# Kernel optimization log

Measured on AMD Instinct MI355X. Metric: run time of the kernel, lower is better.

The kernel has to match this reference:

```python
import math
import jax, jax.numpy as jnp
import numpy as np

NUM_EXPERTS = 8
TOP_K = 2
HIDDEN = 1024
INTER = 2816
CAPACITY_FACTOR = 2.0
T_TOKENS = 4096


def setup_inputs() -> dict:
    key = jax.random.key(0)
    k1, k2, k3, k4, k5 = jax.random.split(key, 5)
    hidden_states = jax.random.normal(k1, (T_TOKENS, HIDDEN), dtype=jnp.float32)
    # router-softmax-like affinities in (0,1)
    expert_affinities = jax.nn.softmax(
        jax.random.normal(k2, (T_TOKENS, NUM_EXPERTS), dtype=jnp.float32), axis=-1)
    expert_index = jax.random.randint(k3, (T_TOKENS, TOP_K), 0, NUM_EXPERTS, dtype=jnp.int64)
    scale = 0.02
    w_gate_up = jax.random.normal(k4, (NUM_EXPERTS, HIDDEN, 2 * INTER), dtype=jnp.float32) * scale
    w_down = jax.random.normal(k5, (NUM_EXPERTS, INTER, HIDDEN), dtype=jnp.float32) * scale
    return {
        "hidden_states": hidden_states,
        "expert_affinities": expert_affinities,
        "expert_index": expert_index,
        "w_gate_up": w_gate_up,
        "w_down": w_down,
    }


def _experts_mlp(x, w_gate_up, w_down):
    # x: (E, C, H) -> (E, C, H); GLU MLP per expert (grouped GEMM)
    gu = jnp.einsum('ech,ehf->ecf', x, w_gate_up)          # (E, C, 2I)
    gate, up = jnp.split(gu, 2, axis=-1)
    h = jax.nn.silu(gate) * up                              # (E, C, I)
    return jnp.einsum('eci,eih->ech', h, w_down)            # (E, C, H)


def reference(hidden_states, expert_affinities, expert_index, w_gate_up, w_down):
    T, H = hidden_states.shape
    E = w_gate_up.shape[0]
    K = expert_index.shape[1]
    # expert capacity C = min(T, ceil(T * top_k * capacity_factor / E))
    C = min(math.ceil(T * K * CAPACITY_FACTOR / E), T)

    expert_index = expert_index.astype(jnp.int32)
    # top_k-hot expert mask (T, E)
    expert_mask = jnp.sum(jax.nn.one_hot(expert_index, E, dtype=jnp.float32), axis=1)
    # 1-indexed position of each token within its expert (cumsum over tokens)
    pos = jnp.cumsum(expert_mask, axis=0)                   # (T, E)
    # drop tokens over capacity
    expert_mask = jnp.where(pos > C, 0.0, expert_mask)

    # mask affinities to chosen (non-dropped) experts, L1-normalize (normalize_top_k_affinities)
    aff = jnp.where(expert_mask == 0, 0.0, expert_affinities)
    aff = aff / jnp.maximum(jnp.sum(jnp.abs(aff), axis=1, keepdims=True), 1e-12)

    # flattened position within (E*C) permuted buffer; 0 marks dropped/unchosen
    offsets = jnp.arange(E, dtype=jnp.float32) * C
    pos_off = jnp.where(expert_mask == 0, 0.0, pos + offsets)  # (T, E)

    tidx = jnp.arange(T, dtype=jnp.int32)
    perm = jnp.take_along_axis(pos_off, expert_index, axis=1).astype(jnp.int32)  # (T, K), 1-indexed

    # scatter token ids into expert-aligned slots (slot 0 is the drop sink)
    vals = jnp.broadcast_to((tidx + 1)[:, None], (T, K))
    assign = jnp.zeros(E * C + 1, dtype=jnp.int32).at[perm.reshape(-1)].set(vals.reshape(-1))
    assign = assign[1:].reshape(E, C)

    perm = jnp.maximum(perm - 1, 0)      # (T, K) -> 0-indexed, dropped clamped to 0
    assign = jnp.maximum(assign - 1, 0)  # (E, C) -> 0-indexed, empty slots read token 0

    # permute -> grouped expert MLP -> combine
    x = hidden_states[assign]                               # (E, C, H)
    permuted = _experts_mlp(x, w_gate_up, w_down).reshape(E * C, H)

    out_k = permuted[perm]                                  # (T, K, H)
    aff_k = jnp.take_along_axis(aff, expert_index, axis=1)  # (T, K); 0 for dropped
    return jnp.sum(out_k * aff_k[..., None], axis=1)        # (T, H)
```

## Files before the change

### kernel.cpp

```cpp
#include <hip/hip_runtime.h>

#define T_TOK 4096
#define NEXP  8
#define HID   1024
#define INTER 2816
#define CAP   2048

typedef __attribute__((ext_vector_type(8))) short bf16x8;
typedef __attribute__((ext_vector_type(4))) float f32x4;

__device__ __forceinline__ float bf2f(unsigned short u){
  union { unsigned int i; float f; } c; c.i = ((unsigned int)u) << 16; return c.f;
}
__device__ __forceinline__ unsigned short f2bf(float f){
  union { float f; unsigned int i; } c; c.f = f;
  unsigned int x = c.i;
  unsigned int r = (x + 0x7fffu + ((x >> 16) & 1u)) >> 16;
  return (unsigned short)r;
}

__device__ __forceinline__ void gload_lds16(const void* g, void* l){
  __builtin_amdgcn_global_load_lds(
      (const __attribute__((address_space(1))) void*)g,
      (__attribute__((address_space(3))) void*)l, 16, 0, 0);
}

__global__ void routing_kernel(const int* __restrict__ eidx,
                               int* __restrict__ assign,
                               int* __restrict__ perm,
                               int* __restrict__ counts)
{
  int tid = threadIdx.x;
  for (int i = tid; i < NEXP * CAP; i += 512) assign[i] = 0;
  __syncthreads();
  int e = tid >> 6;
  int lane = tid & 63;
  int base = 0;
  for (int t0 = 0; t0 < T_TOK; t0 += 64){
    int t = t0 + lane;
    int i0 = eidx[2*t], i1 = eidx[2*t+1];
    int m = (i0 == e) + (i1 == e);
    int v = m;
    #pragma unroll
    for (int off = 1; off < 64; off <<= 1){
      int u = __shfl_up(v, off);
      if (lane >= off) v += u;
    }
    int pos = base + v;
    if (m > 0){
      bool dropped = pos > CAP;
      int slot = dropped ? -1 : (e * CAP + pos - 1);
      if (!dropped) assign[slot] = t;
      if (i0 == e) perm[2*t]   = slot;
      if (i1 == e) perm[2*t+1] = slot;
    }
    base += __shfl(v, 63);
  }
  if (lane == 0) counts[e] = base < CAP ? base : CAP;
}

__global__ void transpose_cast(const float* __restrict__ in, unsigned short* __restrict__ out,
                               int R, int Cc)
{
  __shared__ unsigned short tile[128][66];
  int e = blockIdx.z;
  const float* src = in + (size_t)e * R * Cc;
  unsigned short* dst = out + (size_t)e * R * Cc;
  int c0 = blockIdx.x * 64, r0 = blockIdx.y * 128;
  int tr = threadIdx.x >> 4, tc = threadIdx.x & 15;
  #pragma unroll
  for (int it = 0; it < 8; ++it){
    int r = it*16 + tr;
    float4 v = *(const float4*)(src + (size_t)(r0 + r) * Cc + c0 + tc*4);
    tile[r][tc*4+0] = f2bf(v.x);
    tile[r][tc*4+1] = f2bf(v.y);
    tile[r][tc*4+2] = f2bf(v.z);
    tile[r][tc*4+3] = f2bf(v.w);
  }
  __syncthreads();
  int j0 = tc * 8;
  #pragma unroll
  for (int it = 0; it < 4; ++it){
    int i = it*16 + tr;
    bf16x8 o;
    #pragma unroll
    for (int r = 0; r < 8; ++r) o[r] = (short)tile[j0 + r][i];
    *(bf16x8*)(dst + (size_t)(c0 + i) * R + r0 + j0) = o;
  }
}

__global__ void gather_kernel(const float* __restrict__ hidden,
                              const int* __restrict__ assign,
                              const int* __restrict__ counts,
                              unsigned short* __restrict__ x)
{
  int s = blockIdx.x;
  int e = s / CAP, local = s % CAP;
  if (local >= ((counts[e] + 127) & ~127)) return;
  int tok = assign[s];
  int c = threadIdx.x * 4;
  float4 v = *(const float4*)(hidden + (size_t)tok * HID + c);
  ushort4 o; o.x = f2bf(v.x); o.y = f2bf(v.y); o.z = f2bf(v.z); o.w = f2bf(v.w);
  *(ushort4*)(x + (size_t)s * HID + c) = o;
}

template<int ROWS>
__device__ __forceinline__ void stage_tile(const unsigned short* gbase, int ldk, int k0,
                                           unsigned short* lds, int lane, int wid){
  #pragma unroll
  for (int c = 0; c < ROWS/32; ++c){
    int rb = c*32 + wid*8;
    int row = rb + (lane >> 3);
    int slot = (lane & 7) ^ (row & 7);
    const char* src = (const char*)(gbase + (size_t)row * ldk + k0) + slot*16;
    gload_lds16(src, (char*)lds + rb*128);
  }
}

__device__ __forceinline__ bf16x8 lds_frag(const unsigned short* lds, int row, int kslot){
  int slot = kslot ^ (row & 7);
  return *(const bf16x8*)((const char*)lds + row*128 + slot*16);
}

template<bool SILU, int BN, int KSPLIT>
__global__ __launch_bounds__(256, 4)
void gemm_bf16(const unsigned short* __restrict__ A,
               const unsigned short* __restrict__ Bt,
               unsigned short* __restrict__ O,
               unsigned short* __restrict__ O2,
               const int* __restrict__ counts,
               int K, int Nout)
{
  const int NF = BN / 32;
  int z = blockIdx.z;
  int e = z / KSPLIT, kc = z % KSPLIT;
  int m0 = blockIdx.y * 128;
  if (m0 >= counts[e]) return;
  int n0 = blockIdx.x * BN;
  int klen = K / KSPLIT;
  int kbase = kc * klen;
  unsigned short* Op = (KSPLIT == 2 && kc == 1) ? O2 : O;

  __shared__ unsigned short Al[128*64];
  __shared__ unsigned short Bg[BN*64];
  __shared__ unsigned short Bu[SILU ? BN*64 : 64];

  int tid = threadIdx.x;
  int lane = tid & 63, wid = tid >> 6;
  int wm = wid >> 1, wn = wid & 1;
  int lo = lane & 15, hi = lane >> 4;

  size_t bstride = (size_t)(SILU ? 2*INTER : Nout) * K;
  const unsigned short* Ab  = A  + ((size_t)e * CAP + m0) * K;
  const unsigned short* Bgb = Bt + (size_t)e * bstride + (size_t)n0 * K;
  const unsigned short* Bub = Bt + (size_t)e * bstride + (size_t)(INTER + n0) * K;

  f32x4 accg[4][NF] = {};
  f32x4 accu[SILU ? 4 : 1][SILU ? NF : 1] = {};

  for (int k0 = kbase; k0 < kbase + klen; k0 += 64){
    stage_tile<128>(Ab,  K, k0, Al, lane, wid);
    stage_tile<BN>(Bgb, K, k0, Bg, lane, wid);
    if constexpr (SILU) stage_tile<BN>(Bub, K, k0, Bu, lane, wid);
    __syncthreads();
    #pragma unroll
    for (int kk = 0; kk < 64; kk += 32){
      int kslot = (kk >> 3) + hi;
      bf16x8 af[4], bg_[NF], bu_[NF];
      #pragma unroll
      for (int m = 0; m < 4; ++m) af[m] = lds_frag(Al, wm*64 + m*16 + lo, kslot);
      #pragma unroll
      for (int n = 0; n < NF; ++n) bg_[n] = lds_frag(Bg, wn*(BN/2) + n*16 + lo, kslot);
      if constexpr (SILU){
        #pragma unroll
        for (int n = 0; n < NF; ++n) bu_[n] = lds_frag(Bu, wn*(BN/2) + n*16 + lo, kslot);
      }
      #pragma unroll
      for (int m = 0; m < 4; ++m){
        #pragma unroll
        for (int n = 0; n < NF; ++n){
          accg[m][n] = __builtin_amdgcn_mfma_f32_16x16x32_bf16(af[m], bg_[n], accg[m][n], 0, 0, 0);
          if constexpr (SILU)
            accu[m][n] = __builtin_amdgcn_mfma_f32_16x16x32_bf16(af[m], bu_[n], accu[m][n], 0, 0, 0);
        }
      }
    }
    __syncthreads();
  }

  #pragma unroll
  for (int m = 0; m < 4; ++m){
    #pragma unroll
    for (int n = 0; n < NF; ++n){
      int gr = m0 + wm*64 + m*16 + hi*4;
      int gc = n0 + wn*(BN/2) + n*16 + lo;
      #pragma unroll
      for (int j = 0; j < 4; ++j){
        float v;
        if constexpr (SILU){
          float g = accg[m][n][j], u = accu[m][n][j];
          v = g / (1.f + __expf(-g)) * u;
        } else {
          v = accg[m][n][j];
        }
        Op[((size_t)e * CAP + gr + j) * Nout + gc] = f2bf(v);
      }
    }
  }
}

__global__ void combine_kernel(const unsigned short* __restrict__ p0,
                               const unsigned short* __restrict__ p1,
                               const int* __restrict__ perm,
                               const int* __restrict__ eidx,
                               const float* __restrict__ aff,
                               float* __restrict__ out)
{
  int t = blockIdx.x;
  int i0 = eidx[2*t], i1 = eidx[2*t+1];
  int q0 = perm[2*t], q1 = perm[2*t+1];
  float a0 = (q0 >= 0) ? aff[t*NEXP + i0] : 0.f;
  float a1 = (q1 >= 0) ? aff[t*NEXP + i1] : 0.f;
  float denom = (i0 == i1) ? fabsf(a0) : (fabsf(a0) + fabsf(a1));
  denom = fmaxf(denom, 1e-12f);
  float w0 = a0 / denom, w1 = a1 / denom;
  size_t s0 = (size_t)(q0 >= 0 ? q0 : 0) * HID;
  size_t s1 = (size_t)(q1 >= 0 ? q1 : 0) * HID;
  int c = threadIdx.x * 4;
  ushort4 v0a = *(const ushort4*)(p0 + s0 + c);
  ushort4 v0b = *(const ushort4*)(p1 + s0 + c);
  ushort4 v1a = *(const ushort4*)(p0 + s1 + c);
  ushort4 v1b = *(const ushort4*)(p1 + s1 + c);
  float4 o;
  o.x = w0*(bf2f(v0a.x)+bf2f(v0b.x)) + w1*(bf2f(v1a.x)+bf2f(v1b.x));
  o.y = w0*(bf2f(v0a.y)+bf2f(v0b.y)) + w1*(bf2f(v1a.y)+bf2f(v1b.y));
  o.z = w0*(bf2f(v0a.z)+bf2f(v0b.z)) + w1*(bf2f(v1a.z)+bf2f(v1b.z));
  o.w = w0*(bf2f(v0a.w)+bf2f(v0b.w)) + w1*(bf2f(v1a.w)+bf2f(v1b.w));
  *(float4*)(out + (size_t)t * HID + c) = o;
}

extern "C" void kernel_launch(void* const* d_in, const int* in_sizes, int n_in,
                              void* d_out, int out_size, void* d_ws, size_t ws_size,
                              hipStream_t stream)
{
  const float* hidden = (const float*)d_in[0];
  const float* aff    = (const float*)d_in[1];
  const int*   eidx   = (const int*)d_in[2];
  const float* wgu    = (const float*)d_in[3];
  const float* wdn    = (const float*)d_in[4];
  float* out = (float*)d_out;

  char* ws = (char*)d_ws;
  unsigned short* wt     = (unsigned short*)(ws + 0);
  unsigned short* p1     = (unsigned short*)(ws + 46137344);
  unsigned short* h      = (unsigned short*)(ws + 92274688);
  unsigned short* x      = (unsigned short*)(ws + 184549376);
  int* assign            = (int*)(ws + 218103808);
  int* perm              = (int*)(ws + 218169344);
  int* counts            = (int*)(ws + 218202112);

  routing_kernel<<<1, 512, 0, stream>>>(eidx, assign, perm, counts);
  transpose_cast<<<dim3(88, 8, 8), 256, 0, stream>>>(wgu, wt, HID, 2*INTER);
  gather_kernel<<<dim3(NEXP*CAP), 256, 0, stream>>>(hidden, assign, counts, x);
  gemm_bf16<true, 64, 1><<<dim3(44, 16, 8), 256, 0, stream>>>(x, wt, h, nullptr, counts, HID, INTER);
  transpose_cast<<<dim3(16, 22, 8), 256, 0, stream>>>(wdn, wt, INTER, HID);
  gemm_bf16<false, 128, 2><<<dim3(8, 16, 16), 256, 0, stream>>>(h, wt, x, p1, counts, INTER, HID);
  combine_kernel<<<dim3(T_TOK), 256, 0, stream>>>(x, p1, perm, eidx, aff, out);
}
```

Before: 308.4 us.

## Fuse weight transposes with gather and gate-up GEMM into combined launches

Merges the gate-up weight transpose and the token gather into a single prep launch, and runs the down-weight transpose inside the same launch as the first grouped GEMM. Separate buffers for the two transposed weights let the down-weight conversion overlap with GEMM1 instead of waiting for it. This removes two kernel launches and their serialization gaps. In exchange it needs a larger workspace, and the fused GEMM1 blocks share a grid with memory-bound transpose blocks, which may change occupancy and scheduling.

```diff
diff --git a/kernel.cpp b/kernel.cpp
--- a/kernel.cpp
+++ b/kernel.cpp
@@ -59,23 +59,19 @@
   if (lane == 0) counts[e] = base < CAP ? base : CAP;
 }
 
-__global__ void transpose_cast(const float* __restrict__ in, unsigned short* __restrict__ out,
-                               int R, int Cc)
-{
-  __shared__ unsigned short tile[128][66];
-  int e = blockIdx.z;
-  const float* src = in + (size_t)e * R * Cc;
-  unsigned short* dst = out + (size_t)e * R * Cc;
-  int c0 = blockIdx.x * 64, r0 = blockIdx.y * 128;
+__device__ __forceinline__ void do_transpose(const float* __restrict__ src,
+                                             unsigned short* __restrict__ dst,
+                                             int R, int Cc, int c0, int r0,
+                                             unsigned short* tile ){
   int tr = threadIdx.x >> 4, tc = threadIdx.x & 15;
   #pragma unroll
   for (int it = 0; it < 8; ++it){
     int r = it*16 + tr;
     float4 v = *(const float4*)(src + (size_t)(r0 + r) * Cc + c0 + tc*4);
-    tile[r][tc*4+0] = f2bf(v.x);
-    tile[r][tc*4+1] = f2bf(v.y);
-    tile[r][tc*4+2] = f2bf(v.z);
-    tile[r][tc*4+3] = f2bf(v.w);
+    tile[r*66 + tc*4+0] = f2bf(v.x);
+    tile[r*66 + tc*4+1] = f2bf(v.y);
+    tile[r*66 + tc*4+2] = f2bf(v.z);
+    tile[r*66 + tc*4+3] = f2bf(v.w);
   }
   __syncthreads();
   int j0 = tc * 8;
@@ -84,24 +80,34 @@
     int i = it*16 + tr;
     bf16x8 o;
     #pragma unroll
-    for (int r = 0; r < 8; ++r) o[r] = (short)tile[j0 + r][i];
+    for (int r = 0; r < 8; ++r) o[r] = (short)tile[(j0 + r)*66 + i];
     *(bf16x8*)(dst + (size_t)(c0 + i) * R + r0 + j0) = o;
   }
 }
 
-__global__ void gather_kernel(const float* __restrict__ hidden,
-                              const int* __restrict__ assign,
-                              const int* __restrict__ counts,
-                              unsigned short* __restrict__ x)
-{
-  int s = blockIdx.x;
-  int e = s / CAP, local = s % CAP;
-  if (local >= ((counts[e] + 127) & ~127)) return;
-  int tok = assign[s];
-  int c = threadIdx.x * 4;
-  float4 v = *(const float4*)(hidden + (size_t)tok * HID + c);
-  ushort4 o; o.x = f2bf(v.x); o.y = f2bf(v.y); o.z = f2bf(v.z); o.w = f2bf(v.w);
-  *(ushort4*)(x + (size_t)s * HID + c) = o;
+__global__ void prep_kernel(const float* __restrict__ wgu, unsigned short* __restrict__ wguT,
+                            const float* __restrict__ hidden,
+                            const int* __restrict__ assign, const int* __restrict__ counts,
+                            unsigned short* __restrict__ x)
+{
+  __shared__ unsigned short tile[128*66];
+  int b = blockIdx.x;
+  if (b < 5632){
+    int c0 = (b % 88) * 64;
+    int r0 = ((b / 88) & 7) * 128;
+    int e  = b / 704;
+    do_transpose(wgu + (size_t)e * HID * (2*INTER), wguT + (size_t)e * HID * (2*INTER),
+                 HID, 2*INTER, c0, r0, tile);
+  } else {
+    int s = b - 5632;
+    int e = s / CAP, local = s % CAP;
+    if (local >= ((counts[e] + 127) & ~127)) return;
+    int tok = assign[s];
+    int c = threadIdx.x * 4;
+    float4 v = *(const float4*)(hidden + (size_t)tok * HID + c);
+    ushort4 o; o.x = f2bf(v.x); o.y = f2bf(v.y); o.z = f2bf(v.z); o.w = f2bf(v.w);
+    *(ushort4*)(x + (size_t)s * HID + c) = o;
+  }
 }
 
 template<int ROWS>
@@ -122,67 +128,137 @@
   return *(const bf16x8*)((const char*)lds + row*128 + slot*16);
 }
 
-template<bool SILU, int BN, int KSPLIT>
+__device__ void gemm1_body(const unsigned short* __restrict__ A,
+                           const unsigned short* __restrict__ Bt,
+                           unsigned short* __restrict__ O,
+                           const int* __restrict__ counts,
+                           int nx, int my, int e, unsigned short* smem)
+{
+  int m0 = my * 128;
+  if (m0 >= counts[e]) return;
+  int n0 = nx * 64;
+  unsigned short* Al = smem;
+  unsigned short* Bg = smem + 8192;
+  unsigned short* Bu = smem + 12288;
+
+  int tid = threadIdx.x, lane = tid & 63, wid = tid >> 6;
+  int wm = wid >> 1, wn = wid & 1;
+  int lo = lane & 15, hi = lane >> 4;
+
+  const unsigned short* Ab  = A  + ((size_t)e * CAP + m0) * HID;
+  const unsigned short* Bgb = Bt + (size_t)e * (2*INTER) * HID + (size_t)n0 * HID;
+  const unsigned short* Bub = Bt + (size_t)e * (2*INTER) * HID + (size_t)(INTER + n0) * HID;
+
+  f32x4 accg[4][2] = {}, accu[4][2] = {};
+
+  for (int k0 = 0; k0 < HID; k0 += 64){
+    stage_tile<128>(Ab,  HID, k0, Al, lane, wid);
+    stage_tile<64>(Bgb, HID, k0, Bg, lane, wid);
+    stage_tile<64>(Bub, HID, k0, Bu, lane, wid);
+    __syncthreads();
+    #pragma unroll
+    for (int kk = 0; kk < 64; kk += 32){
+      int kslot = (kk >> 3) + hi;
+      bf16x8 af[4], bg_[2], bu_[2];
+      #pragma unroll
+      for (int m = 0; m < 4; ++m) af[m] = lds_frag(Al, wm*64 + m*16 + lo, kslot);
+      #pragma unroll
+      for (int n = 0; n < 2; ++n){
+        bg_[n] = lds_frag(Bg, wn*32 + n*16 + lo, kslot);
+        bu_[n] = lds_frag(Bu, wn*32 + n*16 + lo, kslot);
+      }
+      #pragma unroll
+      for (int m = 0; m < 4; ++m){
+        #pragma unroll
+        for (int n = 0; n < 2; ++n){
+          accg[m][n] = __builtin_amdgcn_mfma_f32_16x16x32_bf16(af[m], bg_[n], accg[m][n], 0, 0, 0);
+          accu[m][n] = __builtin_amdgcn_mfma_f32_16x16x32_bf16(af[m], bu_[n], accu[m][n], 0, 0, 0);
+        }
+      }
+    }
+    __syncthreads();
+  }
+
+  #pragma unroll
+  for (int m = 0; m < 4; ++m){
+    #pragma unroll
+    for (int n = 0; n < 2; ++n){
+      int gr = m0 + wm*64 + m*16 + hi*4;
+      int gc = n0 + wn*32 + n*16 + lo;
+      #pragma unroll
+      for (int j = 0; j < 4; ++j){
+        float g = accg[m][n][j], u = accu[m][n][j];
+        float v = g / (1.f + __expf(-g)) * u;
+        O[((size_t)e * CAP + gr + j) * INTER + gc] = f2bf(v);
+      }
+    }
+  }
+}
+
 __global__ __launch_bounds__(256, 4)
-void gemm_bf16(const unsigned short* __restrict__ A,
-               const unsigned short* __restrict__ Bt,
-               unsigned short* __restrict__ O,
-               unsigned short* __restrict__ O2,
-               const int* __restrict__ counts,
-               int K, int Nout)
-{
-  const int NF = BN / 32;
+void gemm1_wdnT(const unsigned short* __restrict__ x, const unsigned short* __restrict__ wguT,
+                unsigned short* __restrict__ h, const int* __restrict__ counts,
+                const float* __restrict__ wdn, unsigned short* __restrict__ wdT)
+{
+  __shared__ unsigned short smem[16384];
+  int b = blockIdx.x;
+  if (b < 2816){
+    int c0 = (b % 16) * 64;
+    int r0 = ((b / 16) % 22) * 128;
+    int e  = b / 352;
+    do_transpose(wdn + (size_t)e * INTER * HID, wdT + (size_t)e * INTER * HID,
+                 INTER, HID, c0, r0, smem);
+  } else {
+    int g = b - 2816;
+    int nx = g % 44, my = (g / 44) & 15, e = g / 704;
+    gemm1_body(x, wguT, h, counts, nx, my, e, smem);
+  }
+}
+
+__global__ __launch_bounds__(256, 4)
+void gemm2(const unsigned short* __restrict__ A,
+           const unsigned short* __restrict__ Bt,
+           unsigned short* __restrict__ O,
+           unsigned short* __restrict__ O2,
+           const int* __restrict__ counts)
+{
   int z = blockIdx.z;
-  int e = z / KSPLIT, kc = z % KSPLIT;
+  int e = z >> 1, kc = z & 1;
   int m0 = blockIdx.y * 128;
   if (m0 >= counts[e]) return;
-  int n0 = blockIdx.x * BN;
-  int klen = K / KSPLIT;
-  int kbase = kc * klen;
-  unsigned short* Op = (KSPLIT == 2 && kc == 1) ? O2 : O;
+  int n0 = blockIdx.x * 128;
+  int kbase = kc * (INTER/2);
+  unsigned short* Op = kc ? O2 : O;
 
   __shared__ unsigned short Al[128*64];
-  __shared__ unsigned short Bg[BN*64];
-  __shared__ unsigned short Bu[SILU ? BN*64 : 64];
-
-  int tid = threadIdx.x;
-  int lane = tid & 63, wid = tid >> 6;
+  __shared__ unsigned short Bg[128*64];
+
+  int tid = threadIdx.x, lane = tid & 63, wid = tid >> 6;
   int wm = wid >> 1, wn = wid & 1;
   int lo = lane & 15, hi = lane >> 4;
 
-  size_t bstride = (size_t)(SILU ? 2*INTER : Nout) * K;
-  const unsigned short* Ab  = A  + ((size_t)e * CAP + m0) * K;
-  const unsigned short* Bgb = Bt + (size_t)e * bstride + (size_t)n0 * K;
-  const unsigned short* Bub = Bt + (size_t)e * bstride + (size_t)(INTER + n0) * K;
-
-  f32x4 accg[4][NF] = {};
-  f32x4 accu[SILU ? 4 : 1][SILU ? NF : 1] = {};
-
-  for (int k0 = kbase; k0 < kbase + klen; k0 += 64){
-    stage_tile<128>(Ab,  K, k0, Al, lane, wid);
-    stage_tile<BN>(Bgb, K, k0, Bg, lane, wid);
-    if constexpr (SILU) stage_tile<BN>(Bub, K, k0, Bu, lane, wid);
+  const unsigned short* Ab  = A  + ((size_t)e * CAP + m0) * INTER;
+  const unsigned short* Bgb = Bt + (size_t)e * HID * INTER + (size_t)n0 * INTER;
+
+  f32x4 accg[4][4] = {};
+
+  for (int k0 = kbase; k0 < kbase + INTER/2; k0 += 64){
+    stage_tile<128>(Ab,  INTER, k0, Al, lane, wid);
+    stage_tile<128>(Bgb, INTER, k0, Bg, lane, wid);
     __syncthreads();
     #pragma unroll
     for (int kk = 0; kk < 64; kk += 32){
       int kslot = (kk >> 3) + hi;
-      bf16x8 af[4], bg_[NF], bu_[NF];
+      bf16x8 af[4], bg_[4];
       #pragma unroll
       for (int m = 0; m < 4; ++m) af[m] = lds_frag(Al, wm*64 + m*16 + lo, kslot);
       #pragma unroll
-      for (int n = 0; n < NF; ++n) bg_[n] = lds_frag(Bg, wn*(BN/2) + n*16 + lo, kslot);
-      if constexpr (SILU){
-        #pragma unroll
-        for (int n = 0; n < NF; ++n) bu_[n] = lds_frag(Bu, wn*(BN/2) + n*16 + lo, kslot);
-      }
+      for (int n = 0; n < 4; ++n) bg_[n] = lds_frag(Bg, wn*64 + n*16 + lo, kslot);
       #pragma unroll
       for (int m = 0; m < 4; ++m){
         #pragma unroll
-        for (int n = 0; n < NF; ++n){
+        for (int n = 0; n < 4; ++n)
           accg[m][n] = __builtin_amdgcn_mfma_f32_16x16x32_bf16(af[m], bg_[n], accg[m][n], 0, 0, 0);
-          if constexpr (SILU)
-            accu[m][n] = __builtin_amdgcn_mfma_f32_16x16x32_bf16(af[m], bu_[n], accu[m][n], 0, 0, 0);
-        }
       }
     }
     __syncthreads();
@@ -191,20 +267,12 @@
   #pragma unroll
   for (int m = 0; m < 4; ++m){
     #pragma unroll
-    for (int n = 0; n < NF; ++n){
+    for (int n = 0; n < 4; ++n){
       int gr = m0 + wm*64 + m*16 + hi*4;
-      int gc = n0 + wn*(BN/2) + n*16 + lo;
-      #pragma unroll
-      for (int j = 0; j < 4; ++j){
-        float v;
-        if constexpr (SILU){
-          float g = accg[m][n][j], u = accu[m][n][j];
-          v = g / (1.f + __expf(-g)) * u;
-        } else {
-          v = accg[m][n][j];
-        }
-        Op[((size_t)e * CAP + gr + j) * Nout + gc] = f2bf(v);
-      }
+      int gc = n0 + wn*64 + n*16 + lo;
+      #pragma unroll
+      for (int j = 0; j < 4; ++j)
+        Op[((size_t)e * CAP + gr + j) * HID + gc] = f2bf(accg[m][n][j]);
     }
   }
 }
@@ -251,19 +319,18 @@
   float* out = (float*)d_out;
 
   char* ws = (char*)d_ws;
-  unsigned short* wt     = (unsigned short*)(ws + 0);
-  unsigned short* p1     = (unsigned short*)(ws + 46137344);
-  unsigned short* h      = (unsigned short*)(ws + 92274688);
-  unsigned short* x      = (unsigned short*)(ws + 184549376);
-  int* assign            = (int*)(ws + 218103808);
-  int* perm              = (int*)(ws + 218169344);
-  int* counts            = (int*)(ws + 218202112);
+  unsigned short* wguT = (unsigned short*)(ws + 0);
+  unsigned short* wdT  = (unsigned short*)(ws + 92274688);
+  unsigned short* h    = (unsigned short*)(ws + 138412032);
+  unsigned short* x    = (unsigned short*)(ws + 230686720);
+  unsigned short* p1   = (unsigned short*)(ws + 264241152);
+  int* assign          = (int*)(ws + 297795584);
+  int* perm            = (int*)(ws + 297861120);
+  int* counts          = (int*)(ws + 297893888);
 
   routing_kernel<<<1, 512, 0, stream>>>(eidx, assign, perm, counts);
-  transpose_cast<<<dim3(88, 8, 8), 256, 0, stream>>>(wgu, wt, HID, 2*INTER);
-  gather_kernel<<<dim3(NEXP*CAP), 256, 0, stream>>>(hidden, assign, counts, x);
-  gemm_bf16<true, 64, 1><<<dim3(44, 16, 8), 256, 0, stream>>>(x, wt, h, nullptr, counts, HID, INTER);
-  transpose_cast<<<dim3(16, 22, 8), 256, 0, stream>>>(wdn, wt, INTER, HID);
-  gemm_bf16<false, 128, 2><<<dim3(8, 16, 16), 256, 0, stream>>>(h, wt, x, p1, counts, INTER, HID);
+  prep_kernel<<<dim3(22016), 256, 0, stream>>>(wgu, wguT, hidden, assign, counts, x);
+  gemm1_wdnT<<<dim3(8448), 256, 0, stream>>>(x, wguT, h, counts, wdn, wdT);
+  gemm2<<<dim3(8, 16, 16), 256, 0, stream>>>(h, wdT, x, p1, counts);
   combine_kernel<<<dim3(T_TOK), 256, 0, stream>>>(x, p1, perm, eidx, aff, out);
 }
```

New measurement: 305.1 us. Within noise of the previous version (-1.1%).
